# Optimization experiments

Hardware: AMD Instinct MI355X
Metric: run time of the kernel (lower is better)

The kernel has to match this reference:

```python
import jax, jax.numpy as jnp
import numpy as np

D_MODEL = 1024
HIDDEN = 4096
NUM_EXPERTS = 8
TOP_K = 2
N_TOKENS = 4 * 2048  # batch * seq


def setup_inputs() -> dict:
    key = jax.random.key(0)
    k_x, k_w, k_i, k1, k2, k3 = jax.random.split(key, 6)
    x = jax.random.normal(k_x, (4, 2048, D_MODEL), dtype=jnp.float32)
    expert_weights = jax.random.uniform(k_w, (N_TOKENS, TOP_K), dtype=jnp.float32)
    expert_indices = jax.random.randint(k_i, (N_TOKENS, TOP_K), 0, NUM_EXPERTS)
    scale = 1.0 / np.sqrt(D_MODEL)
    w1 = jax.random.normal(k1, (NUM_EXPERTS, D_MODEL, HIDDEN), dtype=jnp.float32) * scale
    w3 = jax.random.normal(k3, (NUM_EXPERTS, D_MODEL, HIDDEN), dtype=jnp.float32) * scale
    w2 = jax.random.normal(k2, (NUM_EXPERTS, HIDDEN, D_MODEL), dtype=jnp.float32) * (1.0 / np.sqrt(HIDDEN))
    return {"x": x, "expert_weights": expert_weights, "expert_indices": expert_indices,
            "w1": w1, "w2": w2, "w3": w3}


def reference(x, expert_weights, expert_indices, w1, w2, w3):
    # forward_once of ParallelDroplessMLP (single-rank dropless MoE).
    in_shape = x.shape
    d_model = x.shape[-1]
    num_experts = w1.shape[0]
    xf = x.reshape(-1, d_model)                        # (N, d)
    top_k = expert_weights.shape[-1]
    ew = expert_weights.reshape(-1)                    # (N*top_k,)
    ei = expert_indices.reshape(-1).astype(jnp.int32)  # (N*top_k,)

    # indices_and_bins: stable sort by expert id + histogram
    order = jnp.argsort(ei)                            # (T,) permuted row -> flat (token, k) slot
    tokens_per_expert = jnp.bincount(ei, length=num_experts).astype(jnp.int32)

    # gather: replicate each token top_k times, grouped by expert
    token_of_row = order // top_k                      # (T,)
    xg = jnp.take(xf, token_of_row, axis=0)            # (T, d)

    # grouped GEMM (MegaBlocks-style) SwiGLU per expert via ragged_dot
    h = jax.nn.silu(jax.lax.ragged_dot(xg, w1, tokens_per_expert)) \
        * jax.lax.ragged_dot(xg, w3, tokens_per_expert)            # (T, hidden)
    y = jax.lax.ragged_dot(h, w2, tokens_per_expert)               # (T, d)

    # scatter: weighted un-permute back to token positions
    y = y * ew[order][:, None]
    out = jnp.zeros_like(xf).at[token_of_row].add(y)
    return out.reshape(in_shape), tokens_per_expert
```

## Files before the change

kernel.cpp:

```cpp
#include <hip/hip_runtime.h>

#define NTOK 8192
#define TROWS 16384
#define DM 1024
#define HID 4096
#define NEXP 8
#define MAXT256 72
#define MAXT128 136

typedef __bf16 bf16x8 __attribute__((ext_vector_type(8)));
typedef float  f32x4  __attribute__((ext_vector_type(4)));
typedef short  s16x4  __attribute__((ext_vector_type(4)));

#define BAR() do { asm volatile("" ::: "memory"); __builtin_amdgcn_s_barrier(); asm volatile("" ::: "memory"); } while(0)
#define VM6() asm volatile("s_waitcnt vmcnt(6)" ::: "memory")
#define VM0() asm volatile("s_waitcnt vmcnt(0)" ::: "memory")

__device__ __forceinline__ short f2bf(float f) {
  union { float f; unsigned u; } v; v.f = f;
  unsigned r = (v.u + 0x7fffu + ((v.u >> 16) & 1u)) >> 16;
  return (short)r;
}
__device__ __forceinline__ float bf2f(short s) {
  union { unsigned u; float f; } z; z.u = ((unsigned)(unsigned short)s) << 16; return z.f;
}

__device__ __forceinline__ void gload16(const short* g, short* l) {
  __builtin_amdgcn_global_load_lds(
      (const __attribute__((address_space(1))) void*)g,
      (__attribute__((address_space(3))) void*)l, 16, 0, 0);
}

__global__ void k_meta(const int* __restrict__ ei, int* __restrict__ meta,
                       float* __restrict__ outCounts) {
  __shared__ int c[NEXP];
  int tid = threadIdx.x;
  if (tid < NEXP) c[tid] = 0;
  __syncthreads();
  for (int i = tid; i < TROWS; i += 256) atomicAdd(&c[ei[i]], 1);
  __syncthreads();
  if (tid == 0) {
    int off = 0, s = 0, s2 = 0;
    for (int e = 0; e < NEXP; ++e) {
      int ce = c[e];
      meta[e] = ce;
      meta[8 + e] = off;
      meta[16 + e] = off;
      outCounts[e] = (float)ce;
      for (int r0 = 0; r0 < ce; r0 += 256) {
        meta[32 + 3*s] = e; meta[32 + 3*s + 1] = off + r0;
        meta[32 + 3*s + 2] = (ce - r0 < 256) ? (ce - r0) : 256; ++s;
      }
      for (int r0 = 0; r0 < ce; r0 += 128) {
        meta[256 + 3*s2] = e; meta[256 + 3*s2 + 1] = off + r0;
        meta[256 + 3*s2 + 2] = (ce - r0 < 128) ? (ce - r0) : 128; ++s2;
      }
      off += ce;
    }
    for (; s < MAXT256; ++s)  { meta[32 + 3*s] = 0;  meta[32 + 3*s + 1] = 0;  meta[32 + 3*s + 2] = 0; }
    for (; s2 < MAXT128; ++s2){ meta[256 + 3*s2] = 0; meta[256 + 3*s2 + 1] = 0; meta[256 + 3*s2 + 2] = 0; }
  }
}

__global__ void k_scatter(const int* __restrict__ ei, int* __restrict__ meta,
                          int* __restrict__ rowmap, int* __restrict__ inv) {
  int t = blockIdx.x * blockDim.x + threadIdx.x;
  if (t < TROWS) {
    int e = ei[t];
    int p = atomicAdd(&meta[16 + e], 1);
    rowmap[p] = t;
    inv[t] = p;
  }
}

__global__ void k_transpose64(const float* __restrict__ in, short* __restrict__ out,
                              int R, int C) {
  __shared__ float lt[64][65];
  int e = blockIdx.z;
  int c0 = blockIdx.x * 64, r0 = blockIdx.y * 64;
  int t = threadIdx.x;
  int rr = t >> 4, cc = (t & 15) * 4;
  const float* src = in + ((size_t)e * R + r0 + rr) * C + c0 + cc;
#pragma unroll
  for (int i = 0; i < 4; ++i)
    *(f32x4*)&lt[rr + i*16][cc] = *(const f32x4*)(src + (size_t)i * 16 * C);
  __syncthreads();
  int cN = t >> 4, r4 = (t & 15) * 4;
  short* dst = out + ((size_t)e * C + c0 + cN) * R + r0 + r4;
#pragma unroll
  for (int i = 0; i < 4; ++i) {
    s16x4 o;
#pragma unroll
    for (int j = 0; j < 4; ++j) o[j] = f2bf(lt[r4 + j][cN + i*16]);
    *(s16x4*)(dst + (size_t)i * 16 * R) = o;
  }
}

__global__ void k_cvt_x(const float* __restrict__ x, short* __restrict__ xb) {
  const int n4 = NTOK * DM / 4;
  for (int i = blockIdx.x * blockDim.x + threadIdx.x; i < n4; i += gridDim.x * blockDim.x) {
    f32x4 v = ((const f32x4*)x)[i];
    s16x4 s = { f2bf(v.x), f2bf(v.y), f2bf(v.z), f2bf(v.w) };
    ((s16x4*)xb)[i] = s;
  }
}

__global__ __launch_bounds__(512, 2) void k_gemm1(
    const short* __restrict__ xb, const short* __restrict__ w1t, const short* __restrict__ w3t,
    const int* __restrict__ rowmap, const int* __restrict__ meta, short* __restrict__ hbuf) {
  int bid = blockIdx.x;
  int swz = (bid & 7) * 288 + (bid >> 3);
  int slot = swz % MAXT256;
  int bn   = swz / MAXT256;
  int rows = meta[32 + 3*slot + 2];
  if (rows <= 0) return;
  int e    = meta[32 + 3*slot];
  int row0 = meta[32 + 3*slot + 1];

  __shared__ short lA [2][256 * 64];
  __shared__ short lB1[2][128 * 64];
  __shared__ short lB3[2][128 * 64];

  int tid = threadIdx.x, l = tid & 63, w = tid >> 6;
  int wr = (w >> 2) * 128, wc = (w & 3) * 32;
  int lr = l & 15, cb = (l >> 4) * 16, axor = (lr & 7) << 4;
  int srow = l >> 3;
  int scol = ((l & 7) ^ srow) * 8;

  const short* aG[2][2];
#pragma unroll
  for (int h = 0; h < 2; ++h)
#pragma unroll
    for (int i = 0; i < 2; ++i) {
      int r = h*128 + w*16 + i*8 + srow;
      int rc = r < rows ? r : rows - 1;
      int tok = rowmap[row0 + rc] >> 1;
      aG[h][i] = xb + (size_t)tok * DM + scol;
    }
  const short *b1G[2], *b3G[2];
#pragma unroll
  for (int i = 0; i < 2; ++i) {
    size_t grow = (size_t)e * HID + (size_t)bn * 128 + w*16 + i*8 + srow;
    b1G[i] = w1t + grow * DM + scol;
    b3G[i] = w3t + grow * DM + scol;
  }

  f32x4 acc1[2][4][2], acc3[2][4][2];
#pragma unroll
  for (int h = 0; h < 2; ++h)
#pragma unroll
    for (int i = 0; i < 4; ++i)
#pragma unroll
      for (int j = 0; j < 2; ++j) {
        acc1[h][i][j] = (f32x4){0.f,0.f,0.f,0.f};
        acc3[h][i][j] = (f32x4){0.f,0.f,0.f,0.f};
      }

  auto stgA = [&](int buf, int h, int kt) {
    gload16(aG[h][0] + kt, &lA[buf][(h*128 + w*16    ) * 64]);
    gload16(aG[h][1] + kt, &lA[buf][(h*128 + w*16 + 8) * 64]);
  };
  auto stgB1 = [&](int buf, int kt) {
    gload16(b1G[0] + kt, &lB1[buf][(w*16    ) * 64]);
    gload16(b1G[1] + kt, &lB1[buf][(w*16 + 8) * 64]);
  };
  auto stgB3 = [&](int buf, int kt) {
    gload16(b3G[0] + kt, &lB3[buf][(w*16    ) * 64]);
    gload16(b3G[1] + kt, &lB3[buf][(w*16 + 8) * 64]);
  };

  stgA(0, 0, 0); stgA(0, 1, 0); stgB1(0, 0); stgB3(0, 0);
  stgB1(1, 64); stgB3(1, 64); stgA(1, 0, 64);
  VM6();
  BAR();

  const int NT = DM / 64;
  int c = 0;
  for (int t = 0; t < NT; ++t, c ^= 1) {
    int kn  = t*64 + 64;
    int kn2 = t*64 + 128;
    const char* cA  = (const char*)&lA [c][0];
    const char* cB1 = (const char*)&lB1[c][0];
    const char* cB3 = (const char*)&lB3[c][0];

    bf16x8 alo[4][2], b1w[2][2];
#pragma unroll
    for (int i = 0; i < 4; ++i)
#pragma unroll
      for (int kk = 0; kk < 2; ++kk)
        alo[i][kk] = *(const bf16x8*)(cA + (wr + i*16 + lr)*128 + ((kk*64 + cb) ^ axor));
#pragma unroll
    for (int j = 0; j < 2; ++j)
#pragma unroll
      for (int kk = 0; kk < 2; ++kk)
        b1w[j][kk] = *(const bf16x8*)(cB1 + (wc + j*16 + lr)*128 + ((kk*64 + cb) ^ axor));
    if (t + 1 < NT) stgA(c ^ 1, 1, kn);
    BAR();
    __builtin_amdgcn_s_setprio(1);
#pragma unroll
    for (int i = 0; i < 4; ++i)
#pragma unroll
      for (int j = 0; j < 2; ++j)
#pragma unroll
        for (int kk = 0; kk < 2; ++kk)
          acc1[0][i][j] = __builtin_amdgcn_mfma_f32_16x16x32_bf16(alo[i][kk], b1w[j][kk], acc1[0][i][j], 0, 0, 0);
    __builtin_amdgcn_s_setprio(0);
    BAR();

    bf16x8 b3w[2][2];
#pragma unroll
    for (int j = 0; j < 2; ++j)
#pragma unroll
      for (int kk = 0; kk < 2; ++kk)
        b3w[j][kk] = *(const bf16x8*)(cB3 + (wc + j*16 + lr)*128 + ((kk*64 + cb) ^ axor));
    if (t + 2 < NT) stgB1(c, kn2);
    BAR();
    __builtin_amdgcn_s_setprio(1);
#pragma unroll
    for (int i = 0; i < 4; ++i)
#pragma unroll
      for (int j = 0; j < 2; ++j)
#pragma unroll
        for (int kk = 0; kk < 2; ++kk)
          acc3[0][i][j] = __builtin_amdgcn_mfma_f32_16x16x32_bf16(alo[i][kk], b3w[j][kk], acc3[0][i][j], 0, 0, 0);
    __builtin_amdgcn_s_setprio(0);
    BAR();

    bf16x8 ahi[4][2];
#pragma unroll
    for (int i = 0; i < 4; ++i)
#pragma unroll
      for (int kk = 0; kk < 2; ++kk)
        ahi[i][kk] = *(const bf16x8*)(cA + (wr + 64 + i*16 + lr)*128 + ((kk*64 + cb) ^ axor));
    if (t + 2 < NT) stgB3(c, kn2);
    BAR();
    __builtin_amdgcn_s_setprio(1);
#pragma unroll
    for (int i = 0; i < 4; ++i)
#pragma unroll
      for (int j = 0; j < 2; ++j)
#pragma unroll
        for (int kk = 0; kk < 2; ++kk)
          acc1[1][i][j] = __builtin_amdgcn_mfma_f32_16x16x32_bf16(ahi[i][kk], b1w[j][kk], acc1[1][i][j], 0, 0, 0);
    __builtin_amdgcn_s_setprio(0);
    BAR();

    if (t + 2 < NT) stgA(c, 0, kn2);
    __builtin_amdgcn_s_setprio(1);
#pragma unroll
    for (int i = 0; i < 4; ++i)
#pragma unroll
      for (int j = 0; j < 2; ++j)
#pragma unroll
        for (int kk = 0; kk < 2; ++kk)
          acc3[1][i][j] = __builtin_amdgcn_mfma_f32_16x16x32_bf16(ahi[i][kk], b3w[j][kk], acc3[1][i][j], 0, 0, 0);
    __builtin_amdgcn_s_setprio(0);
    if (t < NT - 2) { VM6(); } else { VM0(); }
    BAR();
  }

#pragma unroll
  for (int h = 0; h < 2; ++h)
#pragma unroll
    for (int i = 0; i < 4; ++i)
#pragma unroll
      for (int q = 0; q < 4; ++q) {
        int r = wr + h*64 + i*16 + (l >> 4)*4 + q;
        if (r < rows) {
          size_t base = (size_t)(row0 + r) * HID + (size_t)bn * 128 + wc;
#pragma unroll
          for (int j = 0; j < 2; ++j) {
            float g = acc1[h][i][j][q], u3 = acc3[h][i][j][q];
            float sv = g / (1.f + __expf(-g));
            hbuf[base + j*16 + lr] = f2bf(sv * u3);
          }
        }
      }
}

__global__ __launch_bounds__(256) void k_gemm2(
    const short* __restrict__ hbuf, const short* __restrict__ w2t,
    const int* __restrict__ meta, short* __restrict__ y) {
  int bid = blockIdx.x;
  int swz = (bid & 7) * 136 + (bid >> 3);
  int slot = swz % MAXT128;
  int bn   = swz / MAXT128;
  int rows = meta[256 + 3*slot + 2];
  if (rows <= 0) return;
  int e    = meta[256 + 3*slot];
  int row0 = meta[256 + 3*slot + 1];

  __shared__ short lA[2][128 * 64];
  __shared__ short lB[2][128 * 64];

  int tid = threadIdx.x, l = tid & 63, w = tid >> 6;
  int wr = (w >> 1) * 64, wc = (w & 1) * 64;
  int lr = l & 15, cb = (l >> 4) * 16, axor = (lr & 7) << 4;
  int srow = l >> 3;
  int scol = ((l & 7) ^ srow) * 8;

  const short* aG[4];
#pragma unroll
  for (int g = 0; g < 4; ++g) {
    int r = g*32 + w*8 + srow;
    int rc = r < rows ? r : rows - 1;
    aG[g] = hbuf + (size_t)(row0 + rc) * HID + scol;
  }
  const short* bG[4];
#pragma unroll
  for (int g = 0; g < 4; ++g) {
    size_t grow = (size_t)e * DM + (size_t)bn * 128 + g*32 + w*8 + srow;
    bG[g] = w2t + grow * HID + scol;
  }

  f32x4 acc[4][4];
#pragma unroll
  for (int i = 0; i < 4; ++i)
#pragma unroll
    for (int j = 0; j < 4; ++j) acc[i][j] = (f32x4){0.f,0.f,0.f,0.f};

  auto stgA = [&](int buf, int g, int kt) {
    gload16(aG[g] + kt, &lA[buf][(g*32 + w*8) * 64]);
  };
  auto stgB = [&](int buf, int g, int kt) {
    gload16(bG[g] + kt, &lB[buf][(g*32 + w*8) * 64]);
  };

  stgA(0,0,0); stgA(0,1,0); stgA(0,2,0); stgA(0,3,0);
  stgB(0,0,0); stgB(0,1,0); stgB(0,2,0); stgB(0,3,0);
  stgB(1,0,64); stgB(1,1,64); stgB(1,2,64); stgB(1,3,64);
  stgA(1,0,64); stgA(1,1,64);
  VM6();
  BAR();

  const int NT = HID / 64;
  int c = 0;
  for (int t = 0; t < NT; ++t, c ^= 1) {
    int kn  = t*64 + 64;
    int kn2 = t*64 + 128;
    const char* cA = (const char*)&lA[c][0];
    const char* cB = (const char*)&lB[c][0];

    bf16x8 alo[2][2], blo[2][2];
#pragma unroll
    for (int i = 0; i < 2; ++i)
#pragma unroll
      for (int kk = 0; kk < 2; ++kk)
        alo[i][kk] = *(const bf16x8*)(cA + (wr + i*16 + lr)*128 + ((kk*64 + cb) ^ axor));
#pragma unroll
    for (int j = 0; j < 2; ++j)
#pragma unroll
      for (int kk = 0; kk < 2; ++kk)
        blo[j][kk] = *(const bf16x8*)(cB + (wc + j*16 + lr)*128 + ((kk*64 + cb) ^ axor));
    if (t + 1 < NT) { stgA(c ^ 1, 2, kn); stgA(c ^ 1, 3, kn); }
    BAR();
    __builtin_amdgcn_s_setprio(1);
#pragma unroll
    for (int i = 0; i < 2; ++i)
#pragma unroll
      for (int j = 0; j < 2; ++j)
#pragma unroll
        for (int kk = 0; kk < 2; ++kk)
          acc[i][j] = __builtin_amdgcn_mfma_f32_16x16x32_bf16(alo[i][kk], blo[j][kk], acc[i][j], 0, 0, 0);
    __builtin_amdgcn_s_setprio(0);
    BAR();

    bf16x8 bhi[2][2];
#pragma unroll
    for (int j = 0; j < 2; ++j)
#pragma unroll
      for (int kk = 0; kk < 2; ++kk)
        bhi[j][kk] = *(const bf16x8*)(cB + (wc + (j+2)*16 + lr)*128 + ((kk*64 + cb) ^ axor));
    if (t + 2 < NT) { stgB(c, 0, kn2); stgB(c, 1, kn2); }
    BAR();
    __builtin_amdgcn_s_setprio(1);
#pragma unroll
    for (int i = 0; i < 2; ++i)
#pragma unroll
      for (int j = 0; j < 2; ++j)
#pragma unroll
        for (int kk = 0; kk < 2; ++kk)
          acc[i][j+2] = __builtin_amdgcn_mfma_f32_16x16x32_bf16(alo[i][kk], bhi[j][kk], acc[i][j+2], 0, 0, 0);
    __builtin_amdgcn_s_setprio(0);
    BAR();

    bf16x8 ahi[2][2];
#pragma unroll
    for (int i = 0; i < 2; ++i)
#pragma unroll
      for (int kk = 0; kk < 2; ++kk)
        ahi[i][kk] = *(const bf16x8*)(cA + (wr + (i+2)*16 + lr)*128 + ((kk*64 + cb) ^ axor));
    if (t + 2 < NT) { stgB(c, 2, kn2); stgB(c, 3, kn2); }
    BAR();
    __builtin_amdgcn_s_setprio(1);
#pragma unroll
    for (int i = 0; i < 2; ++i)
#pragma unroll
      for (int j = 0; j < 2; ++j)
#pragma unroll
        for (int kk = 0; kk < 2; ++kk)
          acc[i+2][j] = __builtin_amdgcn_mfma_f32_16x16x32_bf16(ahi[i][kk], blo[j][kk], acc[i+2][j], 0, 0, 0);
    __builtin_amdgcn_s_setprio(0);
    BAR();

    if (t + 2 < NT) { stgA(c, 0, kn2); stgA(c, 1, kn2); }
    __builtin_amdgcn_s_setprio(1);
#pragma unroll
    for (int i = 0; i < 2; ++i)
#pragma unroll
      for (int j = 0; j < 2; ++j)
#pragma unroll
        for (int kk = 0; kk < 2; ++kk)
          acc[i+2][j+2] = __builtin_amdgcn_mfma_f32_16x16x32_bf16(ahi[i][kk], bhi[j][kk], acc[i+2][j+2], 0, 0, 0);
    __builtin_amdgcn_s_setprio(0);
    if (t < NT - 2) { VM6(); } else { VM0(); }
    BAR();
  }

#pragma unroll
  for (int i = 0; i < 4; ++i)
#pragma unroll
    for (int q = 0; q < 4; ++q) {
      int r = wr + i*16 + (l >> 4)*4 + q;
      if (r < rows) {
        size_t obase = (size_t)(row0 + r) * DM + (size_t)bn * 128 + wc;
#pragma unroll
        for (int j = 0; j < 4; ++j)
          y[obase + j*16 + lr] = f2bf(acc[i][j][q]);
      }
    }
}

__global__ void k_unperm(const short* __restrict__ y, const int* __restrict__ inv,
                         const float* __restrict__ ew, float* __restrict__ out) {
  int i = blockIdx.x * 256 + threadIdx.x;
  int tok = i >> 8, c = i & 255;
  int p0 = inv[2*tok], p1 = inv[2*tok + 1];
  float w0 = ew[2*tok], w1v = ew[2*tok + 1];
  s16x4 a = ((const s16x4*)y)[(size_t)p0 * 256 + c];
  s16x4 b = ((const s16x4*)y)[(size_t)p1 * 256 + c];
  f32x4 r;
#pragma unroll
  for (int j = 0; j < 4; ++j) r[j] = w0 * bf2f(a[j]) + w1v * bf2f(b[j]);
  ((f32x4*)out)[i] = r;
}

extern "C" void kernel_launch(void* const* d_in, const int* in_sizes, int n_in,
                              void* d_out, int out_size, void* d_ws, size_t ws_size,
                              hipStream_t stream) {
  const float* x  = (const float*)d_in[0];
  const float* ew = (const float*)d_in[1];
  const int*   ei = (const int*)d_in[2];
  const float* w1 = (const float*)d_in[3];
  const float* w2 = (const float*)d_in[4];
  const float* w3 = (const float*)d_in[5];
  float* out = (float*)d_out;
  char*  ws  = (char*)d_ws;

  short* w1t = (short*)(ws + 0);
  short* w3t = (short*)(ws + 67108864);
  short* w2t = (short*)(ws + 134217728);
  short* xb  = (short*)(ws + 201326592);
  short* hb  = (short*)(ws + 218103808);
  int*   meta   = (int*)(ws + 352321536);
  int*   rowmap = (int*)(ws + 352321536 + 8192);
  int*   inv    = (int*)(ws + 352321536 + 73728);
  short* y      = (short*)(ws + 0);

  k_meta<<<1, 256, 0, stream>>>(ei, meta, out + (size_t)NTOK * DM);
  k_scatter<<<TROWS / 256, 256, 0, stream>>>(ei, meta, rowmap, inv);
  k_transpose64<<<dim3(HID/64, DM/64, NEXP), 256, 0, stream>>>(w1, w1t, DM, HID);
  k_transpose64<<<dim3(HID/64, DM/64, NEXP), 256, 0, stream>>>(w3, w3t, DM, HID);
  k_transpose64<<<dim3(DM/64, HID/64, NEXP), 256, 0, stream>>>(w2, w2t, HID, DM);
  k_cvt_x<<<2048, 256, 0, stream>>>(x, xb);
  k_gemm1<<<MAXT256 * (HID/128), 512, 0, stream>>>(xb, w1t, w3t, rowmap, meta, hb);
  k_gemm2<<<MAXT128 * (DM/128), 256, 0, stream>>>(hb, w2t, meta, y);
  k_unperm<<<NTOK * DM / 4 / 256, 256, 0, stream>>>(y, inv, ew, out);
}
```

Measured before the change: 823.4 us.

## Enlarge gemm2 tiles to 256x128 with 8 waves and fuse prep kernels

The down-projection GEMM now uses 256-row expert tiles with 512-thread blocks (8 waves, each computing 128x32), in place of 128x128 tiles with 4 waves. This reuses the same 256-row slot metadata as gemm1 and halves the number of B-tile (w2) reloads per row. Separately, the three weight transposes and the x conversion are merged into a single launch to cut kernel launch overhead. The larger tiles leave more padding waste on partial expert tiles and produce fewer blocks to spread across the GPU.

```diff
diff --git a/kernel.cpp b/kernel.cpp
--- a/kernel.cpp
+++ b/kernel.cpp
@@ -14,6 +14,7 @@
 
 #define BAR() do { asm volatile("" ::: "memory"); __builtin_amdgcn_s_barrier(); asm volatile("" ::: "memory"); } while(0)
 #define VM6() asm volatile("s_waitcnt vmcnt(6)" ::: "memory")
+#define VM4() asm volatile("s_waitcnt vmcnt(4)" ::: "memory")
 #define VM0() asm volatile("s_waitcnt vmcnt(0)" ::: "memory")
 
 __device__ __forceinline__ short f2bf(float f) {
@@ -40,7 +41,7 @@
   for (int i = tid; i < TROWS; i += 256) atomicAdd(&c[ei[i]], 1);
   __syncthreads();
   if (tid == 0) {
-    int off = 0, s = 0, s2 = 0;
+    int off = 0, s = 0;
     for (int e = 0; e < NEXP; ++e) {
       int ce = c[e];
       meta[e] = ce;
@@ -51,14 +52,9 @@
         meta[32 + 3*s] = e; meta[32 + 3*s + 1] = off + r0;
         meta[32 + 3*s + 2] = (ce - r0 < 256) ? (ce - r0) : 256; ++s;
       }
-      for (int r0 = 0; r0 < ce; r0 += 128) {
-        meta[256 + 3*s2] = e; meta[256 + 3*s2 + 1] = off + r0;
-        meta[256 + 3*s2 + 2] = (ce - r0 < 128) ? (ce - r0) : 128; ++s2;
-      }
       off += ce;
     }
     for (; s < MAXT256; ++s)  { meta[32 + 3*s] = 0;  meta[32 + 3*s + 1] = 0;  meta[32 + 3*s + 2] = 0; }
-    for (; s2 < MAXT128; ++s2){ meta[256 + 3*s2] = 0; meta[256 + 3*s2 + 1] = 0; meta[256 + 3*s2 + 2] = 0; }
   }
 }
 
@@ -73,11 +69,30 @@
   }
 }
 
-__global__ void k_transpose64(const float* __restrict__ in, short* __restrict__ out,
-                              int R, int C) {
+__global__ void k_prep(const float* __restrict__ w1, const float* __restrict__ w3,
+                       const float* __restrict__ w2, const float* __restrict__ x,
+                       short* __restrict__ w1t, short* __restrict__ w3t,
+                       short* __restrict__ w2t, short* __restrict__ xb) {
+  int b = blockIdx.x;
+  int which = b >> 13;
+  if (which == 3) {
+    int i = (b - 24576) * 256 + threadIdx.x;
+    f32x4 v = ((const f32x4*)x)[i];
+    s16x4 s = { f2bf(v.x), f2bf(v.y), f2bf(v.z), f2bf(v.w) };
+    ((s16x4*)xb)[i] = s;
+    return;
+  }
   __shared__ float lt[64][65];
-  int e = blockIdx.z;
-  int c0 = blockIdx.x * 64, r0 = blockIdx.y * 64;
+  int r = b & 8191;
+  const float* in; short* out; int R, C;
+  if (which == 0)      { in = w1; out = w1t; R = DM;  C = HID; }
+  else if (which == 1) { in = w3; out = w3t; R = DM;  C = HID; }
+  else                 { in = w2; out = w2t; R = HID; C = DM;  }
+  int nx = C >> 6;
+  int e = r >> 10;
+  int rem = r & 1023;
+  int c0 = (rem & (nx - 1)) * 64, r0 = (rem / nx) * 64;
+
   int t = threadIdx.x;
   int rr = t >> 4, cc = (t & 15) * 4;
   const float* src = in + ((size_t)e * R + r0 + rr) * C + c0 + cc;
@@ -93,15 +108,6 @@
 #pragma unroll
     for (int j = 0; j < 4; ++j) o[j] = f2bf(lt[r4 + j][cN + i*16]);
     *(s16x4*)(dst + (size_t)i * 16 * R) = o;
-  }
-}
-
-__global__ void k_cvt_x(const float* __restrict__ x, short* __restrict__ xb) {
-  const int n4 = NTOK * DM / 4;
-  for (int i = blockIdx.x * blockDim.x + threadIdx.x; i < n4; i += gridDim.x * blockDim.x) {
-    f32x4 v = ((const f32x4*)x)[i];
-    s16x4 s = { f2bf(v.x), f2bf(v.y), f2bf(v.z), f2bf(v.w) };
-    ((s16x4*)xb)[i] = s;
   }
 }
 
@@ -278,59 +284,63 @@
       }
 }
 
-__global__ __launch_bounds__(256) void k_gemm2(
+__global__ __launch_bounds__(512, 2) void k_gemm2(
     const short* __restrict__ hbuf, const short* __restrict__ w2t,
     const int* __restrict__ meta, short* __restrict__ y) {
   int bid = blockIdx.x;
-  int swz = (bid & 7) * 136 + (bid >> 3);
-  int slot = swz % MAXT128;
-  int bn   = swz / MAXT128;
-  int rows = meta[256 + 3*slot + 2];
+  int swz = (bid & 7) * 72 + (bid >> 3);
+  int slot = swz % MAXT256;
+  int bn   = swz / MAXT256;
+  int rows = meta[32 + 3*slot + 2];
   if (rows <= 0) return;
-  int e    = meta[256 + 3*slot];
-  int row0 = meta[256 + 3*slot + 1];
-
-  __shared__ short lA[2][128 * 64];
+  int e    = meta[32 + 3*slot];
+  int row0 = meta[32 + 3*slot + 1];
+
+  __shared__ short lA[2][256 * 64];
   __shared__ short lB[2][128 * 64];
 
   int tid = threadIdx.x, l = tid & 63, w = tid >> 6;
-  int wr = (w >> 1) * 64, wc = (w & 1) * 64;
+  int wr = (w >> 2) * 128, wc = (w & 3) * 32;
   int lr = l & 15, cb = (l >> 4) * 16, axor = (lr & 7) << 4;
   int srow = l >> 3;
   int scol = ((l & 7) ^ srow) * 8;
 
-  const short* aG[4];
-#pragma unroll
-  for (int g = 0; g < 4; ++g) {
-    int r = g*32 + w*8 + srow;
-    int rc = r < rows ? r : rows - 1;
-    aG[g] = hbuf + (size_t)(row0 + rc) * HID + scol;
-  }
-  const short* bG[4];
-#pragma unroll
-  for (int g = 0; g < 4; ++g) {
-    size_t grow = (size_t)e * DM + (size_t)bn * 128 + g*32 + w*8 + srow;
-    bG[g] = w2t + grow * HID + scol;
-  }
-
-  f32x4 acc[4][4];
-#pragma unroll
-  for (int i = 0; i < 4; ++i)
-#pragma unroll
-    for (int j = 0; j < 4; ++j) acc[i][j] = (f32x4){0.f,0.f,0.f,0.f};
-
-  auto stgA = [&](int buf, int g, int kt) {
-    gload16(aG[g] + kt, &lA[buf][(g*32 + w*8) * 64]);
+  const short* aG[2][2];
+#pragma unroll
+  for (int h = 0; h < 2; ++h)
+#pragma unroll
+    for (int i = 0; i < 2; ++i) {
+      int r = h*128 + w*16 + i*8 + srow;
+      int rc = r < rows ? r : rows - 1;
+      aG[h][i] = hbuf + (size_t)(row0 + rc) * HID + scol;
+    }
+  const short* bG[2];
+#pragma unroll
+  for (int i = 0; i < 2; ++i) {
+    size_t grow = (size_t)e * DM + (size_t)bn * 128 + w*16 + i*8 + srow;
+    bG[i] = w2t + grow * HID + scol;
+  }
+
+  f32x4 acc[2][4][2];
+#pragma unroll
+  for (int h = 0; h < 2; ++h)
+#pragma unroll
+    for (int i = 0; i < 4; ++i)
+#pragma unroll
+      for (int j = 0; j < 2; ++j) acc[h][i][j] = (f32x4){0.f,0.f,0.f,0.f};
+
+  auto stgA = [&](int buf, int h, int kt) {
+    gload16(aG[h][0] + kt, &lA[buf][(h*128 + w*16    ) * 64]);
+    gload16(aG[h][1] + kt, &lA[buf][(h*128 + w*16 + 8) * 64]);
   };
-  auto stgB = [&](int buf, int g, int kt) {
-    gload16(bG[g] + kt, &lB[buf][(g*32 + w*8) * 64]);
+  auto stgB = [&](int buf, int kt) {
+    gload16(bG[0] + kt, &lB[buf][(w*16    ) * 64]);
+    gload16(bG[1] + kt, &lB[buf][(w*16 + 8) * 64]);
   };
 
-  stgA(0,0,0); stgA(0,1,0); stgA(0,2,0); stgA(0,3,0);
-  stgB(0,0,0); stgB(0,1,0); stgB(0,2,0); stgB(0,3,0);
-  stgB(1,0,64); stgB(1,1,64); stgB(1,2,64); stgB(1,3,64);
-  stgA(1,0,64); stgA(1,1,64);
-  VM6();
+  stgA(0, 0, 0); stgA(0, 1, 0); stgB(0, 0);
+  stgB(1, 64); stgA(1, 0, 64);
+  VM4();
   BAR();
 
   const int NT = HID / 64;
@@ -341,9 +351,9 @@
     const char* cA = (const char*)&lA[c][0];
     const char* cB = (const char*)&lB[c][0];
 
-    bf16x8 alo[2][2], blo[2][2];
-#pragma unroll
-    for (int i = 0; i < 2; ++i)
+    bf16x8 alo[4][2], bw[2][2];
+#pragma unroll
+    for (int i = 0; i < 4; ++i)
 #pragma unroll
       for (int kk = 0; kk < 2; ++kk)
         alo[i][kk] = *(const bf16x8*)(cA + (wr + i*16 + lr)*128 + ((kk*64 + cb) ^ axor));
@@ -351,84 +361,63 @@
     for (int j = 0; j < 2; ++j)
 #pragma unroll
       for (int kk = 0; kk < 2; ++kk)
-        blo[j][kk] = *(const bf16x8*)(cB + (wc + j*16 + lr)*128 + ((kk*64 + cb) ^ axor));
-    if (t + 1 < NT) { stgA(c ^ 1, 2, kn); stgA(c ^ 1, 3, kn); }
-    BAR();
-    __builtin_amdgcn_s_setprio(1);
-#pragma unroll
-    for (int i = 0; i < 2; ++i)
+        bw[j][kk] = *(const bf16x8*)(cB + (wc + j*16 + lr)*128 + ((kk*64 + cb) ^ axor));
+    if (t + 1 < NT) stgA(c ^ 1, 1, kn);
+    BAR();
+    __builtin_amdgcn_s_setprio(1);
+#pragma unroll
+    for (int i = 0; i < 4; ++i)
 #pragma unroll
       for (int j = 0; j < 2; ++j)
 #pragma unroll
         for (int kk = 0; kk < 2; ++kk)
-          acc[i][j] = __builtin_amdgcn_mfma_f32_16x16x32_bf16(alo[i][kk], blo[j][kk], acc[i][j], 0, 0, 0);
-    __builtin_amdgcn_s_setprio(0);
-    BAR();
-
-    bf16x8 bhi[2][2];
-#pragma unroll
-    for (int j = 0; j < 2; ++j)
-#pragma unroll
-      for (int kk = 0; kk < 2; ++kk)
-        bhi[j][kk] = *(const bf16x8*)(cB + (wc + (j+2)*16 + lr)*128 + ((kk*64 + cb) ^ axor));
-    if (t + 2 < NT) { stgB(c, 0, kn2); stgB(c, 1, kn2); }
-    BAR();
-    __builtin_amdgcn_s_setprio(1);
-#pragma unroll
-    for (int i = 0; i < 2; ++i)
-#pragma unroll
-      for (int j = 0; j < 2; ++j)
-#pragma unroll
-        for (int kk = 0; kk < 2; ++kk)
-          acc[i][j+2] = __builtin_amdgcn_mfma_f32_16x16x32_bf16(alo[i][kk], bhi[j][kk], acc[i][j+2], 0, 0, 0);
-    __builtin_amdgcn_s_setprio(0);
-    BAR();
-
-    bf16x8 ahi[2][2];
-#pragma unroll
-    for (int i = 0; i < 2; ++i)
-#pragma unroll
-      for (int kk = 0; kk < 2; ++kk)
-        ahi[i][kk] = *(const bf16x8*)(cA + (wr + (i+2)*16 + lr)*128 + ((kk*64 + cb) ^ axor));
-    if (t + 2 < NT) { stgB(c, 2, kn2); stgB(c, 3, kn2); }
-    BAR();
-    __builtin_amdgcn_s_setprio(1);
-#pragma unroll
-    for (int i = 0; i < 2; ++i)
-#pragma unroll
-      for (int j = 0; j < 2; ++j)
-#pragma unroll
-        for (int kk = 0; kk < 2; ++kk)
-          acc[i+2][j] = __builtin_amdgcn_mfma_f32_16x16x32_bf16(ahi[i][kk], blo[j][kk], acc[i+2][j], 0, 0, 0);
-    __builtin_amdgcn_s_setprio(0);
-    BAR();
-
-    if (t + 2 < NT) { stgA(c, 0, kn2); stgA(c, 1, kn2); }
-    __builtin_amdgcn_s_setprio(1);
-#pragma unroll
-    for (int i = 0; i < 2; ++i)
-#pragma unroll
-      for (int j = 0; j < 2; ++j)
-#pragma unroll
-        for (int kk = 0; kk < 2; ++kk)
-          acc[i+2][j+2] = __builtin_amdgcn_mfma_f32_16x16x32_bf16(ahi[i][kk], bhi[j][kk], acc[i+2][j+2], 0, 0, 0);
-    __builtin_amdgcn_s_setprio(0);
-    if (t < NT - 2) { VM6(); } else { VM0(); }
-    BAR();
-  }
-
-#pragma unroll
-  for (int i = 0; i < 4; ++i)
-#pragma unroll
-    for (int q = 0; q < 4; ++q) {
-      int r = wr + i*16 + (l >> 4)*4 + q;
-      if (r < rows) {
-        size_t obase = (size_t)(row0 + r) * DM + (size_t)bn * 128 + wc;
-#pragma unroll
-        for (int j = 0; j < 4; ++j)
-          y[obase + j*16 + lr] = f2bf(acc[i][j][q]);
+          acc[0][i][j] = __builtin_amdgcn_mfma_f32_16x16x32_bf16(alo[i][kk], bw[j][kk], acc[0][i][j], 0, 0, 0);
+    __builtin_amdgcn_s_setprio(0);
+    BAR();
+
+    bf16x8 ahi[4][2];
+#pragma unroll
+    for (int i = 0; i < 4; ++i)
+#pragma unroll
+      for (int kk = 0; kk < 2; ++kk)
+        ahi[i][kk] = *(const bf16x8*)(cA + (wr + 64 + i*16 + lr)*128 + ((kk*64 + cb) ^ axor));
+    if (t + 2 < NT) stgB(c, kn2);
+    BAR();
+    __builtin_amdgcn_s_setprio(1);
+#pragma unroll
+    for (int i = 0; i < 4; ++i)
+#pragma unroll
+      for (int j = 0; j < 2; ++j)
+        acc[1][i][j] = __builtin_amdgcn_mfma_f32_16x16x32_bf16(ahi[i][0], bw[j][0], acc[1][i][j], 0, 0, 0);
+    __builtin_amdgcn_s_setprio(0);
+    BAR();
+
+    if (t + 2 < NT) stgA(c, 0, kn2);
+    __builtin_amdgcn_s_setprio(1);
+#pragma unroll
+    for (int i = 0; i < 4; ++i)
+#pragma unroll
+      for (int j = 0; j < 2; ++j)
+        acc[1][i][j] = __builtin_amdgcn_mfma_f32_16x16x32_bf16(ahi[i][1], bw[j][1], acc[1][i][j], 0, 0, 0);
+    __builtin_amdgcn_s_setprio(0);
+    if (t < NT - 2) { VM4(); } else { VM0(); }
+    BAR();
+  }
+
+#pragma unroll
+  for (int h = 0; h < 2; ++h)
+#pragma unroll
+    for (int i = 0; i < 4; ++i)
+#pragma unroll
+      for (int q = 0; q < 4; ++q) {
+        int r = wr + h*64 + i*16 + (l >> 4)*4 + q;
+        if (r < rows) {
+          size_t base = (size_t)(row0 + r) * DM + (size_t)bn * 128 + wc;
+#pragma unroll
+          for (int j = 0; j < 2; ++j)
+            y[base + j*16 + lr] = f2bf(acc[h][i][j][q]);
+        }
       }
-    }
 }
 
 __global__ void k_unperm(const short* __restrict__ y, const int* __restrict__ inv,
@@ -469,11 +458,8 @@
 
   k_meta<<<1, 256, 0, stream>>>(ei, meta, out + (size_t)NTOK * DM);
   k_scatter<<<TROWS / 256, 256, 0, stream>>>(ei, meta, rowmap, inv);
-  k_transpose64<<<dim3(HID/64, DM/64, NEXP), 256, 0, stream>>>(w1, w1t, DM, HID);
-  k_transpose64<<<dim3(HID/64, DM/64, NEXP), 256, 0, stream>>>(w3, w3t, DM, HID);
-  k_transpose64<<<dim3(DM/64, HID/64, NEXP), 256, 0, stream>>>(w2, w2t, HID, DM);
-  k_cvt_x<<<2048, 256, 0, stream>>>(x, xb);
+  k_prep<<<32768, 256, 0, stream>>>(w1, w3, w2, x, w1t, w3t, w2t, xb);
   k_gemm1<<<MAXT256 * (HID/128), 512, 0, stream>>>(xb, w1t, w3t, rowmap, meta, hb);
-  k_gemm2<<<MAXT128 * (DM/128), 256, 0, stream>>>(hb, w2t, meta, y);
+  k_gemm2<<<MAXT256 * (DM/128), 512, 0, stream>>>(hb, w2t, meta, y);
   k_unperm<<<NTOK * DM / 4 / 256, 256, 0, stream>>>(y, inv, ew, out);
 }
```

Result: faster. 806.8 us (-2.0%).
